# Optimization experiments

Measured on AMD Instinct MI355X. Metric: run time of the kernel, lower is better.

The kernel has to match this reference:

```python
import jax, jax.numpy as jnp
import numpy as np

B, N, D, H, S = 4, 32768, 256, 8, 64
DH = D // H  # 32


def setup_inputs() -> dict:
    key = jax.random.key(0)
    ks = jax.random.split(key, 8)
    s = 0.02
    return {
        "x": jax.random.normal(ks[0], (B, N, D), jnp.float32),
        "W_fx": jax.random.normal(ks[1], (D, D), jnp.float32) * s,
        "b_fx": jnp.zeros((D,), jnp.float32),
        "W_x": jax.random.normal(ks[2], (D, D), jnp.float32) * s,
        "b_x": jnp.zeros((D,), jnp.float32),
        "W_slice": jax.random.normal(ks[3], (DH, S), jnp.float32) * s,
        "b_slice": jnp.zeros((S,), jnp.float32),
        "temperature": jnp.full((1, H, 1, 1), 0.5, jnp.float32),
        "W_qkv": jax.random.normal(ks[4], (DH, 3 * DH), jnp.float32) * s,  # qkv_bias=False
        "W_out": jax.random.normal(ks[5], (D, D), jnp.float32) * s,
        "b_out": jnp.zeros((D,), jnp.float32),
    }


def reference(x, W_fx, b_fx, W_x, b_x, W_slice, b_slice, temperature, W_qkv, W_out, b_out):
    b, n, d = x.shape
    h, dh = H, d // H
    scale = dh ** -0.5
    # per-head projections: [b, h, n, dh]
    fx_mid = (x @ W_fx + b_fx).reshape(b, n, h, dh).transpose(0, 2, 1, 3)
    x_mid = (x @ W_x + b_x).reshape(b, n, h, dh).transpose(0, 2, 1, 3)
    # soft slice assignment: softmax over slices [b, h, n, s]
    logits = (x_mid @ W_slice + b_slice) / temperature
    slice_weights = jax.nn.softmax(logits, axis=-1)
    slice_norm = slice_weights.sum(axis=2)  # [b, h, s]
    # weighted pooling of points into slice tokens [b, h, s, dh]
    slice_token = jnp.einsum('bhnc,bhns->bhsc', fx_mid, slice_weights)
    slice_token = slice_token / (slice_norm[..., None] + 1e-5)
    # tiny attention among slice tokens
    q, k, v = jnp.split(slice_token @ W_qkv, 3, axis=-1)
    dots = jnp.einsum('bhsc,bhtc->bhst', q, k) * scale
    attn = jax.nn.softmax(dots, axis=-1)
    out_slice_token = attn @ v  # [b, h, s, dh]
    # scatter back to points [b, h, n, dh]
    out_x = jnp.einsum('bhsc,bhns->bhnc', out_slice_token, slice_weights)
    out_x = out_x.transpose(0, 2, 1, 3).reshape(b, n, d)
    return out_x @ W_out + b_out
```

## Files before the change

### kernel.cpp

```cpp
#include <hip/hip_runtime.h>
#include <math.h>

#define TS_N 32768
#define TS_M 131072

typedef short bf16x8 __attribute__((ext_vector_type(8)));
typedef float f32x4  __attribute__((ext_vector_type(4)));
typedef unsigned short us4 __attribute__((ext_vector_type(4)));
typedef unsigned short us8 __attribute__((ext_vector_type(8)));

static __device__ __forceinline__ unsigned short f2bf(float f) {
    unsigned u = __float_as_uint(f);
    u = u + 0x7FFF + ((u >> 16) & 1);
    return (unsigned short)(u >> 16);
}
static __device__ __forceinline__ float bf2f(unsigned short b) {
    return __uint_as_float(((unsigned)b) << 16);
}

#define GL16(gp, lp) __builtin_amdgcn_global_load_lds( \
    (const __attribute__((address_space(1))) unsigned int*)(gp), \
    (__attribute__((address_space(3))) unsigned int*)(lp), 16, 0, 0)

__global__ __launch_bounds__(256) void k0_wt(
    const float* __restrict__ Wfx, const float* __restrict__ Wx,
    unsigned short* __restrict__ Wth, unsigned short* __restrict__ Wtl)
{
    const int n = blockIdx.x;
    const int wsel = blockIdx.y;
    const int k = threadIdx.x;
    const float v = (wsel ? Wx : Wfx)[k * 256 + n];
    const unsigned short hh = f2bf(v);
    const int idx = (wsel * 256 + n) * 256 + k;
    Wth[idx] = hh;
    Wtl[idx] = f2bf(v - bf2f(hh));
}

__global__ __launch_bounds__(256) void k1_gemm(
    const float* __restrict__ x,
    const unsigned short* __restrict__ Wth, const unsigned short* __restrict__ Wtl,
    const float* __restrict__ bfx, const float* __restrict__ bx,
    float* __restrict__ FX, float* __restrict__ XM)
{
    __shared__ unsigned short AldsH[4096];
    __shared__ unsigned short AldsL[4096];
    __shared__ unsigned short BldsH[4096];
    __shared__ unsigned short BldsL[4096];

    const int L = blockIdx.x;
    const int xcd = L & 7, ii = L >> 3;
    const int rb = xcd * 128 + (ii >> 2), nsel = ii & 3;
    const int row0 = rb * 128;
    const int n0 = (nsel & 1) * 128;
    const unsigned short* Bth = Wth + (nsel >> 1) * 65536 + n0 * 256;
    const unsigned short* Btl = Wtl + (nsel >> 1) * 65536 + n0 * 256;
    const float* bias = (nsel >> 1) ? bx : bfx;
    float* OUT = (nsel >> 1) ? XM : FX;

    const int t = threadIdx.x;
    const int w = t >> 6, l = t & 63;
    const int wm = w >> 1, wn = w & 1;
    const int lr = l & 15, lk = l >> 4;

    f32x4 acc[4][4];
#pragma unroll
    for (int i = 0; i < 4; ++i)
#pragma unroll
        for (int j = 0; j < 4; ++j) {
            acc[i][j][0] = 0.f; acc[i][j][1] = 0.f;
            acc[i][j][2] = 0.f; acc[i][j][3] = 0.f;
        }

    for (int step = 0; step < 8; ++step) {
        const int kk = step * 32;
        if (step > 0) __syncthreads();
#pragma unroll
        for (int g2i = 0; g2i < 2; ++g2i) {
            const int g2 = w + g2i * 4;
            const size_t br = (size_t)(g2 * 16 + lr) * 256 + kk + lk * 8;
            const int lb = g2 * 512;
            GL16(Bth + br, BldsH + lb);
            GL16(Btl + br, BldsL + lb);
        }
#pragma unroll
        for (int g2i = 0; g2i < 2; ++g2i) {
            const int g2 = w + g2i * 4;
            const float* ap = &x[(size_t)(row0 + g2 * 16 + lr) * 256 + kk + lk * 8];
            float4 a0 = *(const float4*)ap;
            float4 a1 = *(const float4*)(ap + 4);
            float cc[8] = {a0.x, a0.y, a0.z, a0.w, a1.x, a1.y, a1.z, a1.w};
            us8 vh, vl;
#pragma unroll
            for (int j = 0; j < 8; ++j) {
                const unsigned short hb = f2bf(cc[j]);
                vh[j] = hb;
                vl[j] = f2bf(cc[j] - bf2f(hb));
            }
            *(us8*)&AldsH[(g2 * 64 + l) * 8] = vh;
            *(us8*)&AldsL[(g2 * 64 + l) * 8] = vl;
        }
        __syncthreads();

        bf16x8 ah[4], al[4], bh[4], bl[4];
#pragma unroll
        for (int g = 0; g < 4; ++g) {
            const int ac = (((wm * 4 + g) * 4 + lk) * 16 + lr) * 8;
            ah[g] = *(const bf16x8*)&AldsH[ac];
            al[g] = *(const bf16x8*)&AldsL[ac];
            const int bc = (((wn * 4 + g) * 4 + lk) * 16 + lr) * 8;
            bh[g] = *(const bf16x8*)&BldsH[bc];
            bl[g] = *(const bf16x8*)&BldsL[bc];
        }
#pragma unroll
        for (int m = 0; m < 4; ++m)
#pragma unroll
            for (int n = 0; n < 4; ++n) {
                acc[m][n] = __builtin_amdgcn_mfma_f32_16x16x32_bf16(ah[m], bh[n], acc[m][n], 0, 0, 0);
                acc[m][n] = __builtin_amdgcn_mfma_f32_16x16x32_bf16(ah[m], bl[n], acc[m][n], 0, 0, 0);
                acc[m][n] = __builtin_amdgcn_mfma_f32_16x16x32_bf16(al[m], bh[n], acc[m][n], 0, 0, 0);
            }
    }

    float bv[4];
#pragma unroll
    for (int n = 0; n < 4; ++n) bv[n] = bias[n0 + wn * 64 + n * 16 + lr];
#pragma unroll
    for (int m = 0; m < 4; ++m)
#pragma unroll
        for (int n = 0; n < 4; ++n) {
            const int col = n0 + wn * 64 + n * 16 + lr;
#pragma unroll
            for (int r = 0; r < 4; ++r) {
                const int row = row0 + wm * 64 + m * 16 + lk * 4 + r;
                OUT[(size_t)row * 256 + col] = acc[m][n][r] + bv[n];
            }
        }
}

__global__ __launch_bounds__(256) void k1b_slice_softmax(
    const float* __restrict__ XM, const float* __restrict__ Wsl,
    const float* __restrict__ bsl, const float* __restrict__ temp,
    float* __restrict__ SW)
{
    __shared__ float XMs[32][68];
    __shared__ float Ws[32][68];
    __shared__ float Ls[64][68];
    const int t  = threadIdx.x;
    const int r0 = blockIdx.x * 64;
    const int h  = blockIdx.y;

    {
        const int m = t >> 2, cq = (t & 3) * 8;
        float4 v0 = *(const float4*)&XM[(size_t)(r0 + m) * 256 + h * 32 + cq];
        float4 v1 = *(const float4*)&XM[(size_t)(r0 + m) * 256 + h * 32 + cq + 4];
        XMs[cq + 0][m] = v0.x; XMs[cq + 1][m] = v0.y; XMs[cq + 2][m] = v0.z; XMs[cq + 3][m] = v0.w;
        XMs[cq + 4][m] = v1.x; XMs[cq + 5][m] = v1.y; XMs[cq + 6][m] = v1.z; XMs[cq + 7][m] = v1.w;
        const int wk = t >> 3, wn = (t & 7) * 8;
        float4 u0 = *(const float4*)&Wsl[wk * 64 + wn];
        float4 u1 = *(const float4*)&Wsl[wk * 64 + wn + 4];
        *(float4*)&Ws[wk][wn]     = u0;
        *(float4*)&Ws[wk][wn + 4] = u1;
    }
    __syncthreads();

    const int tx = t & 15, ty = t >> 4;
    float acc[4][4];
#pragma unroll
    for (int i = 0; i < 4; ++i)
#pragma unroll
        for (int j = 0; j < 4; ++j) acc[i][j] = 0.f;
#pragma unroll
    for (int c = 0; c < 32; ++c) {
        float4 av = *(const float4*)&XMs[c][ty * 4];
        float4 bv = *(const float4*)&Ws[c][tx * 4];
        float a_[4] = {av.x, av.y, av.z, av.w};
        float b_[4] = {bv.x, bv.y, bv.z, bv.w};
#pragma unroll
        for (int i = 0; i < 4; ++i)
#pragma unroll
            for (int j = 0; j < 4; ++j)
                acc[i][j] = fmaf(a_[i], b_[j], acc[i][j]);
    }
    const float invt = 1.0f / temp[h];
#pragma unroll
    for (int i = 0; i < 4; ++i)
#pragma unroll
        for (int j = 0; j < 4; ++j)
            Ls[ty * 4 + i][tx * 4 + j] = (acc[i][j] + bsl[tx * 4 + j]) * invt;
    __syncthreads();

    const int row = t >> 2, j4 = t & 3;
    float v[16];
    float mx = -1e30f;
#pragma unroll
    for (int i = 0; i < 16; ++i) { v[i] = Ls[row][j4 * 16 + i]; mx = fmaxf(mx, v[i]); }
    mx = fmaxf(mx, __shfl_xor(mx, 1));
    mx = fmaxf(mx, __shfl_xor(mx, 2));
    float sum = 0.f;
#pragma unroll
    for (int i = 0; i < 16; ++i) { v[i] = expf(v[i] - mx); sum += v[i]; }
    sum += __shfl_xor(sum, 1);
    sum += __shfl_xor(sum, 2);
    const float inv = 1.0f / sum;
#pragma unroll
    for (int q = 0; q < 4; ++q) {
        float4 ov;
        ov.x = v[q * 4 + 0] * inv; ov.y = v[q * 4 + 1] * inv;
        ov.z = v[q * 4 + 2] * inv; ov.w = v[q * 4 + 3] * inv;
        *(float4*)&SW[(size_t)(r0 + row) * 512 + h * 64 + j4 * 16 + q * 4] = ov;
    }
}

__global__ __launch_bounds__(256) void k2_pool(
    const float* __restrict__ FX, const float* __restrict__ SW,
    float* __restrict__ PART, float* __restrict__ PARTN)
{
    __shared__ float SWs[2][64][68];
    __shared__ float FXs[2][64][36];
    const int t = threadIdx.x;
    const int chunk = blockIdx.x;
    const int bh = blockIdx.y;
    const int b = bh >> 3, h = bh & 7;
    const int gbase = b * TS_N + chunk * 512;

    const int rs = t >> 2;
    const int ch0 = t & 3;

    float4 swr[4];
    float4 fxr[2];

    {
        const size_t swbase = (size_t)(gbase + rs) * 512 + h * 64;
        swr[0] = *(const float4*)&SW[swbase + ch0 * 8];
        swr[1] = *(const float4*)&SW[swbase + ch0 * 8 + 4];
        swr[2] = *(const float4*)&SW[swbase + (ch0 + 4) * 8];
        swr[3] = *(const float4*)&SW[swbase + (ch0 + 4) * 8 + 4];
        const size_t fxbase = (size_t)(gbase + rs) * 256 + h * 32;
        fxr[0] = *(const float4*)&FX[fxbase + ch0 * 4];
        fxr[1] = *(const float4*)&FX[fxbase + (ch0 + 4) * 4];
    }

    const int c = t & 31, sb = (t >> 5) * 8;
    float acc[8];
#pragma unroll
    for (int j = 0; j < 8; ++j) acc[j] = 0.f;
    float accn = 0.f;
    int buf = 0;

    for (int s = 0; s < 8; ++s) {
        *(float4*)&SWs[buf][rs][ch0 * 8]           = swr[0];
        *(float4*)&SWs[buf][rs][ch0 * 8 + 4]       = swr[1];
        *(float4*)&SWs[buf][rs][(ch0 + 4) * 8]     = swr[2];
        *(float4*)&SWs[buf][rs][(ch0 + 4) * 8 + 4] = swr[3];
        *(float4*)&FXs[buf][rs][ch0 * 4]       = fxr[0];
        *(float4*)&FXs[buf][rs][(ch0 + 4) * 4] = fxr[1];
        __syncthreads();
        if (s < 7) {
            const int g2 = gbase + (s + 1) * 64 + rs;
            const size_t swbase = (size_t)g2 * 512 + h * 64;
            swr[0] = *(const float4*)&SW[swbase + ch0 * 8];
            swr[1] = *(const float4*)&SW[swbase + ch0 * 8 + 4];
            swr[2] = *(const float4*)&SW[swbase + (ch0 + 4) * 8];
            swr[3] = *(const float4*)&SW[swbase + (ch0 + 4) * 8 + 4];
            const size_t fxbase = (size_t)g2 * 256 + h * 32;
            fxr[0] = *(const float4*)&FX[fxbase + ch0 * 4];
            fxr[1] = *(const float4*)&FX[fxbase + (ch0 + 4) * 4];
        }
#pragma unroll 8
        for (int rr = 0; rr < 64; ++rr) {
            const float f = FXs[buf][rr][c];
            float4 s0 = *(const float4*)&SWs[buf][rr][sb];
            float4 s1 = *(const float4*)&SWs[buf][rr][sb + 4];
            acc[0] = fmaf(f, s0.x, acc[0]); acc[1] = fmaf(f, s0.y, acc[1]);
            acc[2] = fmaf(f, s0.z, acc[2]); acc[3] = fmaf(f, s0.w, acc[3]);
            acc[4] = fmaf(f, s1.x, acc[4]); acc[5] = fmaf(f, s1.y, acc[5]);
            acc[6] = fmaf(f, s1.z, acc[6]); acc[7] = fmaf(f, s1.w, acc[7]);
        }
        if (t < 64) {
#pragma unroll 8
            for (int rr = 0; rr < 64; ++rr) accn += SWs[buf][rr][t];
        }
        buf ^= 1;
    }

    const int pbase = (bh * 64 + chunk) * 2048;
#pragma unroll
    for (int j = 0; j < 8; ++j) PART[pbase + (sb + j) * 32 + c] = acc[j];
    if (t < 64) PARTN[(bh * 64 + chunk) * 64 + t] = accn;
}

__global__ __launch_bounds__(256) void k2b_reduce(
    const float* __restrict__ PART, const float* __restrict__ PARTN,
    float* __restrict__ ST, float* __restrict__ NORM)
{
    const int g = blockIdx.x, bh = blockIdx.y, t = threadIdx.x;
    const int e = g * 256 + t;
    float s = 0.f;
    for (int ch = 0; ch < 64; ++ch) s += PART[(size_t)(bh * 64 + ch) * 2048 + e];
    ST[bh * 2048 + e] = s;
    if (g == 0 && t < 64) {
        float sn = 0.f;
        for (int ch = 0; ch < 64; ++ch) sn += PARTN[(bh * 64 + ch) * 64 + t];
        NORM[bh * 64 + t] = sn;
    }
}

__global__ __launch_bounds__(64) void k3_attn(
    const float* __restrict__ ST, const float* __restrict__ NORM,
    const float* __restrict__ Wqkv, float* __restrict__ OST)
{
    __shared__ float Wq[32 * 96];
    __shared__ float Kl[64][32];
    __shared__ float Vl[64][32];
    __shared__ float Dl[64][68];
    const int bh = blockIdx.x;
    const int s  = threadIdx.x;

    for (int i = 0; i < 48; ++i) Wq[i * 64 + s] = Wqkv[i * 64 + s];
    float st[32];
    const float nrm = NORM[bh * 64 + s] + 1e-5f;
#pragma unroll
    for (int c = 0; c < 32; ++c) st[c] = ST[bh * 2048 + s * 32 + c] / nrm;
    __syncthreads();

    float q[32];
#pragma unroll
    for (int o4 = 0; o4 < 8; ++o4) {
        float ax = 0.f, ay = 0.f, az = 0.f, aw = 0.f;
#pragma unroll
        for (int c = 0; c < 32; ++c) {
            float4 w = *(const float4*)&Wq[c * 96 + o4 * 4];
            ax = fmaf(st[c], w.x, ax); ay = fmaf(st[c], w.y, ay);
            az = fmaf(st[c], w.z, az); aw = fmaf(st[c], w.w, aw);
        }
        q[o4 * 4 + 0] = ax; q[o4 * 4 + 1] = ay; q[o4 * 4 + 2] = az; q[o4 * 4 + 3] = aw;
    }
#pragma unroll
    for (int o4 = 0; o4 < 8; ++o4) {
        float ax = 0.f, ay = 0.f, az = 0.f, aw = 0.f;
#pragma unroll
        for (int c = 0; c < 32; ++c) {
            float4 w = *(const float4*)&Wq[c * 96 + 32 + o4 * 4];
            ax = fmaf(st[c], w.x, ax); ay = fmaf(st[c], w.y, ay);
            az = fmaf(st[c], w.z, az); aw = fmaf(st[c], w.w, aw);
        }
        float4 kv; kv.x = ax; kv.y = ay; kv.z = az; kv.w = aw;
        *(float4*)&Kl[s][o4 * 4] = kv;
    }
#pragma unroll
    for (int o4 = 0; o4 < 8; ++o4) {
        float ax = 0.f, ay = 0.f, az = 0.f, aw = 0.f;
#pragma unroll
        for (int c = 0; c < 32; ++c) {
            float4 w = *(const float4*)&Wq[c * 96 + 64 + o4 * 4];
            ax = fmaf(st[c], w.x, ax); ay = fmaf(st[c], w.y, ay);
            az = fmaf(st[c], w.z, az); aw = fmaf(st[c], w.w, aw);
        }
        float4 vv; vv.x = ax; vv.y = ay; vv.z = az; vv.w = aw;
        *(float4*)&Vl[s][o4 * 4] = vv;
    }
    __syncthreads();

    const float scale = 0.17677669529663687f;
    float mx = -1e30f;
    for (int t2 = 0; t2 < 64; ++t2) {
        float d = 0.f;
#pragma unroll
        for (int c4 = 0; c4 < 8; ++c4) {
            float4 kv = *(const float4*)&Kl[t2][c4 * 4];
            d = fmaf(q[c4 * 4 + 0], kv.x, d); d = fmaf(q[c4 * 4 + 1], kv.y, d);
            d = fmaf(q[c4 * 4 + 2], kv.z, d); d = fmaf(q[c4 * 4 + 3], kv.w, d);
        }
        d *= scale;
        Dl[s][t2] = d;
        mx = fmaxf(mx, d);
    }
    float sum = 0.f;
    for (int t2 = 0; t2 < 64; ++t2) { float e = expf(Dl[s][t2] - mx); Dl[s][t2] = e; sum += e; }
    const float inv = 1.0f / sum;
    float out[32];
#pragma unroll
    for (int c = 0; c < 32; ++c) out[c] = 0.f;
    for (int t2 = 0; t2 < 64; ++t2) {
        const float p = Dl[s][t2] * inv;
#pragma unroll
        for (int c4 = 0; c4 < 8; ++c4) {
            float4 vv = *(const float4*)&Vl[t2][c4 * 4];
            out[c4 * 4 + 0] = fmaf(p, vv.x, out[c4 * 4 + 0]);
            out[c4 * 4 + 1] = fmaf(p, vv.y, out[c4 * 4 + 1]);
            out[c4 * 4 + 2] = fmaf(p, vv.z, out[c4 * 4 + 2]);
            out[c4 * 4 + 3] = fmaf(p, vv.w, out[c4 * 4 + 3]);
        }
    }
#pragma unroll
    for (int c4 = 0; c4 < 8; ++c4) {
        float4 ov;
        ov.x = out[c4 * 4 + 0]; ov.y = out[c4 * 4 + 1];
        ov.z = out[c4 * 4 + 2]; ov.w = out[c4 * 4 + 3];
        *(float4*)&OST[bh * 2048 + s * 32 + c4 * 4] = ov;
    }
}

__global__ __launch_bounds__(256) void k3b_precomb(
    const float* __restrict__ OST, const float* __restrict__ Wout,
    unsigned short* __restrict__ Gth, unsigned short* __restrict__ Gtl)
{
    __shared__ float OSTs[64][36];
    __shared__ float Wc[32][256];
    const int bh = blockIdx.x;
    const int b = bh >> 3, h = bh & 7;
    const int t = threadIdx.x;

#pragma unroll
    for (int j = 0; j < 2; ++j) {
        const int e = (j * 256 + t) * 4;
        float4 v = *(const float4*)&OST[bh * 2048 + e];
        const int s = e >> 5, c = e & 31;
        OSTs[s][c + 0] = v.x; OSTs[s][c + 1] = v.y;
        OSTs[s][c + 2] = v.z; OSTs[s][c + 3] = v.w;
    }
#pragma unroll
    for (int j = 0; j < 8; ++j) {
        const int e = (j * 256 + t) * 4;
        const int c = e >> 8, o = e & 255;
        *(float4*)&Wc[c][o] = *(const float4*)&Wout[(h * 32 + c) * 256 + o];
    }
    __syncthreads();

    float wcol[32];
#pragma unroll
    for (int c = 0; c < 32; ++c) wcol[c] = Wc[c][t];

    for (int s = 0; s < 64; ++s) {
        float a = 0.f;
#pragma unroll
        for (int c = 0; c < 32; ++c) a = fmaf(OSTs[s][c], wcol[c], a);
        const unsigned short gh = f2bf(a);
        const size_t idx = ((size_t)(b * 256 + t)) * 512 + h * 64 + s;
        Gth[idx] = gh;
        Gtl[idx] = f2bf(a - bf2f(gh));
    }
}

__global__ __launch_bounds__(256) void k4_gemm(
    const float* __restrict__ SW,
    const unsigned short* __restrict__ Gth, const unsigned short* __restrict__ Gtl,
    const float* __restrict__ bout, float* __restrict__ out)
{
    __shared__ unsigned short AldsH[4096];
    __shared__ unsigned short AldsL[4096];
    __shared__ unsigned short BldsH[4096];
    __shared__ unsigned short BldsL[4096];
    const int L = blockIdx.x;
    const int xcd = L & 7, ii = L >> 3;
    const int rb = xcd * 128 + (ii >> 1), nsel = ii & 1;
    const int row0 = rb * 128;
    const int n0 = nsel * 128;
    const int b = row0 >> 15;
    const unsigned short* Bth = Gth + ((size_t)b * 256 + n0) * 512;
    const unsigned short* Btl = Gtl + ((size_t)b * 256 + n0) * 512;

    const int t = threadIdx.x;
    const int w = t >> 6, l = t & 63;
    const int wm = w >> 1, wn = w & 1;
    const int lr = l & 15, lk = l >> 4;

    f32x4 acc[4][4];
#pragma unroll
    for (int i = 0; i < 4; ++i)
#pragma unroll
        for (int j = 0; j < 4; ++j) {
            acc[i][j][0] = 0.f; acc[i][j][1] = 0.f;
            acc[i][j][2] = 0.f; acc[i][j][3] = 0.f;
        }

    for (int step = 0; step < 16; ++step) {
        const int kk = step * 32;
        if (step > 0) __syncthreads();
#pragma unroll
        for (int g2i = 0; g2i < 2; ++g2i) {
            const int g2 = w + g2i * 4;
            const size_t br = (size_t)(g2 * 16 + lr) * 512 + kk + lk * 8;
            const int lb = g2 * 512;
            GL16(Bth + br, BldsH + lb);
            GL16(Btl + br, BldsL + lb);
        }
#pragma unroll
        for (int g2i = 0; g2i < 2; ++g2i) {
            const int g2 = w + g2i * 4;
            const float* ap = &SW[(size_t)(row0 + g2 * 16 + lr) * 512 + kk + lk * 8];
            float4 a0 = *(const float4*)ap;
            float4 a1 = *(const float4*)(ap + 4);
            float cc[8] = {a0.x, a0.y, a0.z, a0.w, a1.x, a1.y, a1.z, a1.w};
            us8 vh, vl;
#pragma unroll
            for (int j = 0; j < 8; ++j) {
                const unsigned short hb = f2bf(cc[j]);
                vh[j] = hb;
                vl[j] = f2bf(cc[j] - bf2f(hb));
            }
            *(us8*)&AldsH[(g2 * 64 + l) * 8] = vh;
            *(us8*)&AldsL[(g2 * 64 + l) * 8] = vl;
        }
        __syncthreads();

        bf16x8 ah[4], al[4], bh[4], bl[4];
#pragma unroll
        for (int g = 0; g < 4; ++g) {
            const int ac = (((wm * 4 + g) * 4 + lk) * 16 + lr) * 8;
            ah[g] = *(const bf16x8*)&AldsH[ac];
            al[g] = *(const bf16x8*)&AldsL[ac];
            const int bc = (((wn * 4 + g) * 4 + lk) * 16 + lr) * 8;
            bh[g] = *(const bf16x8*)&BldsH[bc];
            bl[g] = *(const bf16x8*)&BldsL[bc];
        }
#pragma unroll
        for (int m = 0; m < 4; ++m)
#pragma unroll
            for (int n = 0; n < 4; ++n) {
                acc[m][n] = __builtin_amdgcn_mfma_f32_16x16x32_bf16(ah[m], bh[n], acc[m][n], 0, 0, 0);
                acc[m][n] = __builtin_amdgcn_mfma_f32_16x16x32_bf16(ah[m], bl[n], acc[m][n], 0, 0, 0);
                acc[m][n] = __builtin_amdgcn_mfma_f32_16x16x32_bf16(al[m], bh[n], acc[m][n], 0, 0, 0);
            }
    }

    float bv[4];
#pragma unroll
    for (int n = 0; n < 4; ++n) bv[n] = bout[n0 + wn * 64 + n * 16 + lr];
#pragma unroll
    for (int m = 0; m < 4; ++m)
#pragma unroll
        for (int n = 0; n < 4; ++n) {
            const int col = n0 + wn * 64 + n * 16 + lr;
#pragma unroll
            for (int r = 0; r < 4; ++r) {
                const int row = row0 + wm * 64 + m * 16 + lk * 4 + r;
                out[(size_t)row * 256 + col] = acc[m][n][r] + bv[n];
            }
        }
}

extern "C" void kernel_launch(void* const* d_in, const int* in_sizes, int n_in,
                              void* d_out, int out_size, void* d_ws, size_t ws_size,
                              hipStream_t stream) {
    (void)in_sizes; (void)n_in; (void)out_size; (void)ws_size;
    const float* x    = (const float*)d_in[0];
    const float* Wfx  = (const float*)d_in[1];
    const float* bfx  = (const float*)d_in[2];
    const float* Wx   = (const float*)d_in[3];
    const float* bx   = (const float*)d_in[4];
    const float* Wsl  = (const float*)d_in[5];
    const float* bsl  = (const float*)d_in[6];
    const float* temp = (const float*)d_in[7];
    const float* Wqkv = (const float*)d_in[8];
    const float* Wout = (const float*)d_in[9];
    const float* bout = (const float*)d_in[10];
    float* out = (float*)d_out;
    char* w = (char*)d_ws;

    float* XM = (float*)w;
    float* SW = (float*)(w + 134217728);
    char* p = w + 134217728 + 268435456;
    float* ST    = (float*)p;            p += 262144;
    float* NORM  = (float*)p;            p += 8192;
    float* OST   = (float*)p;            p += 262144;
    unsigned short* Gth = (unsigned short*)p; p += 1048576;
    unsigned short* Gtl = (unsigned short*)p; p += 1048576;
    unsigned short* Wth = (unsigned short*)p; p += 262144;
    unsigned short* Wtl = (unsigned short*)p; p += 262144;
    float* PART  = XM;
    float* PARTN = XM + 4194304;
    float* FX = out;

    k0_wt<<<dim3(256, 2), 256, 0, stream>>>(Wfx, Wx, Wth, Wtl);
    k1_gemm<<<4096, 256, 0, stream>>>(x, Wth, Wtl, bfx, bx, FX, XM);
    k1b_slice_softmax<<<dim3(TS_M / 64, 8), 256, 0, stream>>>(XM, Wsl, bsl, temp, SW);
    k2_pool<<<dim3(64, 32), 256, 0, stream>>>(FX, SW, PART, PARTN);
    k2b_reduce<<<dim3(8, 32), 256, 0, stream>>>(PART, PARTN, ST, NORM);
    k3_attn<<<32, 64, 0, stream>>>(ST, NORM, Wqkv, OST);
    k3b_precomb<<<32, 256, 0, stream>>>(OST, Wout, Gth, Gtl);
    k4_gemm<<<2048, 256, 0, stream>>>(SW, Gth, Gtl, bout, out);
}
```

Measured before the change: 612.3 us.

## Fuse partial reduction, slice attention and output precombine into one kernel

Merges the partial-sum reduction, the tiny per-head slice attention, and the Wout precombine into a single 32-block kernel that keeps slice tokens and norms in shared memory. This removes two kernel launches and the global round trips for ST, NORM and OST. In exchange, the reduction over 64 partial chunks now runs on only 32 blocks instead of 256, which lowers parallelism in that phase. The attention part still uses only 64 of 256 threads.

```diff
diff --git a/kernel.cpp b/kernel.cpp
--- a/kernel.cpp
+++ b/kernel.cpp
@@ -289,152 +289,124 @@
     if (t < 64) PARTN[(bh * 64 + chunk) * 64 + t] = accn;
 }
 
-__global__ __launch_bounds__(256) void k2b_reduce(
+__global__ __launch_bounds__(256) void k23_fused(
     const float* __restrict__ PART, const float* __restrict__ PARTN,
-    float* __restrict__ ST, float* __restrict__ NORM)
+    const float* __restrict__ Wqkv, const float* __restrict__ Wout,
+    unsigned short* __restrict__ Gth, unsigned short* __restrict__ Gtl)
 {
-    const int g = blockIdx.x, bh = blockIdx.y, t = threadIdx.x;
-    const int e = g * 256 + t;
-    float s = 0.f;
-    for (int ch = 0; ch < 64; ++ch) s += PART[(size_t)(bh * 64 + ch) * 2048 + e];
-    ST[bh * 2048 + e] = s;
-    if (g == 0 && t < 64) {
-        float sn = 0.f;
-        for (int ch = 0; ch < 64; ++ch) sn += PARTN[(bh * 64 + ch) * 64 + t];
-        NORM[bh * 64 + t] = sn;
-    }
-}
-
-__global__ __launch_bounds__(64) void k3_attn(
-    const float* __restrict__ ST, const float* __restrict__ NORM,
-    const float* __restrict__ Wqkv, float* __restrict__ OST)
-{
+    __shared__ float STl[2048];
+    __shared__ float NORMs[64];
     __shared__ float Wq[32 * 96];
     __shared__ float Kl[64][32];
     __shared__ float Vl[64][32];
     __shared__ float Dl[64][68];
     const int bh = blockIdx.x;
-    const int s  = threadIdx.x;
-
-    for (int i = 0; i < 48; ++i) Wq[i * 64 + s] = Wqkv[i * 64 + s];
-    float st[32];
-    const float nrm = NORM[bh * 64 + s] + 1e-5f;
-#pragma unroll
-    for (int c = 0; c < 32; ++c) st[c] = ST[bh * 2048 + s * 32 + c] / nrm;
-    __syncthreads();
-
-    float q[32];
-#pragma unroll
-    for (int o4 = 0; o4 < 8; ++o4) {
-        float ax = 0.f, ay = 0.f, az = 0.f, aw = 0.f;
-#pragma unroll
-        for (int c = 0; c < 32; ++c) {
-            float4 w = *(const float4*)&Wq[c * 96 + o4 * 4];
-            ax = fmaf(st[c], w.x, ax); ay = fmaf(st[c], w.y, ay);
-            az = fmaf(st[c], w.z, az); aw = fmaf(st[c], w.w, aw);
-        }
-        q[o4 * 4 + 0] = ax; q[o4 * 4 + 1] = ay; q[o4 * 4 + 2] = az; q[o4 * 4 + 3] = aw;
-    }
-#pragma unroll
-    for (int o4 = 0; o4 < 8; ++o4) {
-        float ax = 0.f, ay = 0.f, az = 0.f, aw = 0.f;
-#pragma unroll
-        for (int c = 0; c < 32; ++c) {
-            float4 w = *(const float4*)&Wq[c * 96 + 32 + o4 * 4];
-            ax = fmaf(st[c], w.x, ax); ay = fmaf(st[c], w.y, ay);
-            az = fmaf(st[c], w.z, az); aw = fmaf(st[c], w.w, aw);
-        }
-        float4 kv; kv.x = ax; kv.y = ay; kv.z = az; kv.w = aw;
-        *(float4*)&Kl[s][o4 * 4] = kv;
-    }
-#pragma unroll
-    for (int o4 = 0; o4 < 8; ++o4) {
-        float ax = 0.f, ay = 0.f, az = 0.f, aw = 0.f;
-#pragma unroll
-        for (int c = 0; c < 32; ++c) {
-            float4 w = *(const float4*)&Wq[c * 96 + 64 + o4 * 4];
-            ax = fmaf(st[c], w.x, ax); ay = fmaf(st[c], w.y, ay);
-            az = fmaf(st[c], w.z, az); aw = fmaf(st[c], w.w, aw);
-        }
-        float4 vv; vv.x = ax; vv.y = ay; vv.z = az; vv.w = aw;
-        *(float4*)&Vl[s][o4 * 4] = vv;
-    }
-    __syncthreads();
-
-    const float scale = 0.17677669529663687f;
-    float mx = -1e30f;
-    for (int t2 = 0; t2 < 64; ++t2) {
-        float d = 0.f;
-#pragma unroll
-        for (int c4 = 0; c4 < 8; ++c4) {
-            float4 kv = *(const float4*)&Kl[t2][c4 * 4];
-            d = fmaf(q[c4 * 4 + 0], kv.x, d); d = fmaf(q[c4 * 4 + 1], kv.y, d);
-            d = fmaf(q[c4 * 4 + 2], kv.z, d); d = fmaf(q[c4 * 4 + 3], kv.w, d);
-        }
-        d *= scale;
-        Dl[s][t2] = d;
-        mx = fmaxf(mx, d);
-    }
-    float sum = 0.f;
-    for (int t2 = 0; t2 < 64; ++t2) { float e = expf(Dl[s][t2] - mx); Dl[s][t2] = e; sum += e; }
-    const float inv = 1.0f / sum;
-    float out[32];
-#pragma unroll
-    for (int c = 0; c < 32; ++c) out[c] = 0.f;
-    for (int t2 = 0; t2 < 64; ++t2) {
-        const float p = Dl[s][t2] * inv;
-#pragma unroll
-        for (int c4 = 0; c4 < 8; ++c4) {
-            float4 vv = *(const float4*)&Vl[t2][c4 * 4];
-            out[c4 * 4 + 0] = fmaf(p, vv.x, out[c4 * 4 + 0]);
-            out[c4 * 4 + 1] = fmaf(p, vv.y, out[c4 * 4 + 1]);
-            out[c4 * 4 + 2] = fmaf(p, vv.z, out[c4 * 4 + 2]);
-            out[c4 * 4 + 3] = fmaf(p, vv.w, out[c4 * 4 + 3]);
-        }
-    }
-#pragma unroll
-    for (int c4 = 0; c4 < 8; ++c4) {
-        float4 ov;
-        ov.x = out[c4 * 4 + 0]; ov.y = out[c4 * 4 + 1];
-        ov.z = out[c4 * 4 + 2]; ov.w = out[c4 * 4 + 3];
-        *(float4*)&OST[bh * 2048 + s * 32 + c4 * 4] = ov;
-    }
-}
-
-__global__ __launch_bounds__(256) void k3b_precomb(
-    const float* __restrict__ OST, const float* __restrict__ Wout,
-    unsigned short* __restrict__ Gth, unsigned short* __restrict__ Gtl)
-{
-    __shared__ float OSTs[64][36];
-    __shared__ float Wc[32][256];
-    const int bh = blockIdx.x;
     const int b = bh >> 3, h = bh & 7;
     const int t = threadIdx.x;
 
 #pragma unroll
-    for (int j = 0; j < 2; ++j) {
-        const int e = (j * 256 + t) * 4;
-        float4 v = *(const float4*)&OST[bh * 2048 + e];
-        const int s = e >> 5, c = e & 31;
-        OSTs[s][c + 0] = v.x; OSTs[s][c + 1] = v.y;
-        OSTs[s][c + 2] = v.z; OSTs[s][c + 3] = v.w;
-    }
-#pragma unroll
     for (int j = 0; j < 8; ++j) {
-        const int e = (j * 256 + t) * 4;
-        const int c = e >> 8, o = e & 255;
-        *(float4*)&Wc[c][o] = *(const float4*)&Wout[(h * 32 + c) * 256 + o];
-    }
+        const int e = j * 256 + t;
+        float s = 0.f;
+        for (int ch = 0; ch < 64; ++ch) s += PART[(size_t)(bh * 64 + ch) * 2048 + e];
+        STl[e] = s;
+    }
+    if (t < 64) {
+        float sn = 0.f;
+        for (int ch = 0; ch < 64; ++ch) sn += PARTN[(bh * 64 + ch) * 64 + t];
+        NORMs[t] = sn;
+    }
+#pragma unroll
+    for (int j = 0; j < 12; ++j) Wq[j * 256 + t] = Wqkv[j * 256 + t];
     __syncthreads();
 
+    if (t < 64) {
+        const int s = t;
+        float st[32];
+        const float nrm = NORMs[s] + 1e-5f;
+#pragma unroll
+        for (int c = 0; c < 32; ++c) st[c] = STl[s * 32 + c] / nrm;
+
+        float q[32];
+#pragma unroll
+        for (int o4 = 0; o4 < 8; ++o4) {
+            float ax = 0.f, ay = 0.f, az = 0.f, aw = 0.f;
+#pragma unroll
+            for (int c = 0; c < 32; ++c) {
+                float4 w = *(const float4*)&Wq[c * 96 + o4 * 4];
+                ax = fmaf(st[c], w.x, ax); ay = fmaf(st[c], w.y, ay);
+                az = fmaf(st[c], w.z, az); aw = fmaf(st[c], w.w, aw);
+            }
+            q[o4 * 4 + 0] = ax; q[o4 * 4 + 1] = ay; q[o4 * 4 + 2] = az; q[o4 * 4 + 3] = aw;
+        }
+#pragma unroll
+        for (int o4 = 0; o4 < 8; ++o4) {
+            float ax = 0.f, ay = 0.f, az = 0.f, aw = 0.f;
+#pragma unroll
+            for (int c = 0; c < 32; ++c) {
+                float4 w = *(const float4*)&Wq[c * 96 + 32 + o4 * 4];
+                ax = fmaf(st[c], w.x, ax); ay = fmaf(st[c], w.y, ay);
+                az = fmaf(st[c], w.z, az); aw = fmaf(st[c], w.w, aw);
+            }
+            float4 kv; kv.x = ax; kv.y = ay; kv.z = az; kv.w = aw;
+            *(float4*)&Kl[s][o4 * 4] = kv;
+        }
+#pragma unroll
+        for (int o4 = 0; o4 < 8; ++o4) {
+            float ax = 0.f, ay = 0.f, az = 0.f, aw = 0.f;
+#pragma unroll
+            for (int c = 0; c < 32; ++c) {
+                float4 w = *(const float4*)&Wq[c * 96 + 64 + o4 * 4];
+                ax = fmaf(st[c], w.x, ax); ay = fmaf(st[c], w.y, ay);
+                az = fmaf(st[c], w.z, az); aw = fmaf(st[c], w.w, aw);
+            }
+            float4 vv; vv.x = ax; vv.y = ay; vv.z = az; vv.w = aw;
+            *(float4*)&Vl[s][o4 * 4] = vv;
+        }
+        const float scale = 0.17677669529663687f;
+        float mx = -1e30f;
+        for (int t2 = 0; t2 < 64; ++t2) {
+            float d = 0.f;
+#pragma unroll
+            for (int c4 = 0; c4 < 8; ++c4) {
+                float4 kv = *(const float4*)&Kl[t2][c4 * 4];
+                d = fmaf(q[c4 * 4 + 0], kv.x, d); d = fmaf(q[c4 * 4 + 1], kv.y, d);
+                d = fmaf(q[c4 * 4 + 2], kv.z, d); d = fmaf(q[c4 * 4 + 3], kv.w, d);
+            }
+            d *= scale;
+            Dl[s][t2] = d;
+            mx = fmaxf(mx, d);
+        }
+        float sum = 0.f;
+        for (int t2 = 0; t2 < 64; ++t2) { float e = expf(Dl[s][t2] - mx); Dl[s][t2] = e; sum += e; }
+        const float inv = 1.0f / sum;
+        float outv[32];
+#pragma unroll
+        for (int c = 0; c < 32; ++c) outv[c] = 0.f;
+        for (int t2 = 0; t2 < 64; ++t2) {
+            const float p = Dl[s][t2] * inv;
+#pragma unroll
+            for (int c4 = 0; c4 < 8; ++c4) {
+                float4 vv = *(const float4*)&Vl[t2][c4 * 4];
+                outv[c4 * 4 + 0] = fmaf(p, vv.x, outv[c4 * 4 + 0]);
+                outv[c4 * 4 + 1] = fmaf(p, vv.y, outv[c4 * 4 + 1]);
+                outv[c4 * 4 + 2] = fmaf(p, vv.z, outv[c4 * 4 + 2]);
+                outv[c4 * 4 + 3] = fmaf(p, vv.w, outv[c4 * 4 + 3]);
+            }
+        }
+#pragma unroll
+        for (int c = 0; c < 32; ++c) STl[s * 32 + c] = outv[c];
+    }
+    __syncthreads();
+
     float wcol[32];
 #pragma unroll
-    for (int c = 0; c < 32; ++c) wcol[c] = Wc[c][t];
+    for (int c = 0; c < 32; ++c) wcol[c] = Wout[(h * 32 + c) * 256 + t];
 
     for (int s = 0; s < 64; ++s) {
         float a = 0.f;
 #pragma unroll
-        for (int c = 0; c < 32; ++c) a = fmaf(OSTs[s][c], wcol[c], a);
+        for (int c = 0; c < 32; ++c) a = fmaf(STl[s * 32 + c], wcol[c], a);
         const unsigned short gh = f2bf(a);
         const size_t idx = ((size_t)(b * 256 + t)) * 512 + h * 64 + s;
         Gth[idx] = gh;
@@ -561,9 +533,6 @@
     float* XM = (float*)w;
     float* SW = (float*)(w + 134217728);
     char* p = w + 134217728 + 268435456;
-    float* ST    = (float*)p;            p += 262144;
-    float* NORM  = (float*)p;            p += 8192;
-    float* OST   = (float*)p;            p += 262144;
     unsigned short* Gth = (unsigned short*)p; p += 1048576;
     unsigned short* Gtl = (unsigned short*)p; p += 1048576;
     unsigned short* Wth = (unsigned short*)p; p += 262144;
@@ -576,8 +545,6 @@
     k1_gemm<<<4096, 256, 0, stream>>>(x, Wth, Wtl, bfx, bx, FX, XM);
     k1b_slice_softmax<<<dim3(TS_M / 64, 8), 256, 0, stream>>>(XM, Wsl, bsl, temp, SW);
     k2_pool<<<dim3(64, 32), 256, 0, stream>>>(FX, SW, PART, PARTN);
-    k2b_reduce<<<dim3(8, 32), 256, 0, stream>>>(PART, PARTN, ST, NORM);
-    k3_attn<<<32, 64, 0, stream>>>(ST, NORM, Wqkv, OST);
-    k3b_precomb<<<32, 256, 0, stream>>>(OST, Wout, Gth, Gtl);
+    k23_fused<<<32, 256, 0, stream>>>(PART, PARTN, Wqkv, Wout, Gth, Gtl);
     k4_gemm<<<2048, 256, 0, stream>>>(SW, Gth, Gtl, bout, out);
 }
```

Result: slower. 630.5 us (+3.0%).
